# Optimization experiments

Hardware: AMD Instinct MI355X
Metric: run time of the kernel (lower is better)

The kernel has to match this reference:

```python
import jax, jax.numpy as jnp
import numpy as np

SCALE = 0.2  # init_kwargs: scale
EPS = 1e-12  # F.normalize default eps


def setup_inputs() -> dict:
    key = jax.random.key(0)
    x = jax.random.normal(key, (8, 2048, 512), dtype=jnp.float32)
    return {"x": x}


def reference(x):
    # x: [B, N, D]
    # F.normalize(x, dim=2): x / max(||x||_2, eps)
    norm = jnp.linalg.norm(x, axis=2, keepdims=True)
    x_norm = x / jnp.maximum(norm, EPS)
    # sim: [B, N, N] = x_norm @ x_norm^T, softmax over last dim
    sim = jnp.einsum('bnd,bmd->bnm', x_norm, x_norm)
    attn = jax.nn.softmax(sim, axis=2)
    # (1 + scale) * x - scale * attn @ x
    out = (1.0 + SCALE) * x - SCALE * jnp.einsum('bnm,bmd->bnd', attn, x)
    return out
```

## Files before the change

### kernel.cpp

```cpp
#include <hip/hip_runtime.h>
#include <stdint.h>

typedef unsigned short ushort_t;
typedef float f32x4 __attribute__((ext_vector_type(4)));
typedef short bf16x8 __attribute__((ext_vector_type(8)));
typedef unsigned short us8 __attribute__((ext_vector_type(8)));

#define BATCH 8
#define SEQ   2048
#define DIM   512
#define MBLK  64
#define KBLK  32
#define NIT   (SEQ / KBLK)

__device__ __forceinline__ ushort_t f2bf(float f) {
  union { float f; uint32_t u; } c; c.f = f;
  uint32_t u = c.u;
  uint32_t r = (u + 0x7FFFu + ((u >> 16) & 1u)) >> 16;
  return (ushort_t)r;
}
__device__ __forceinline__ uint32_t packbf(float a, float b) {
  return (uint32_t)f2bf(a) | ((uint32_t)f2bf(b) << 16);
}
__device__ __forceinline__ void gload_lds16(const void* g, void* l) {
  __builtin_amdgcn_global_load_lds(
      (const __attribute__((address_space(1))) unsigned int*)g,
      (__attribute__((address_space(3))) unsigned int*)l, 16, 0, 0);
}

__global__ void k_norm(const float* __restrict__ x, ushort_t* __restrict__ xn) {
  const int lane = threadIdx.x & 63;
  const int wid  = threadIdx.x >> 6;
  const size_t row = (size_t)blockIdx.x * 4 + wid;
  const float* xr = x + row * DIM;
  const float4 a = ((const float4*)xr)[lane * 2];
  const float4 b = ((const float4*)xr)[lane * 2 + 1];
  float ss = a.x*a.x + a.y*a.y + a.z*a.z + a.w*a.w
           + b.x*b.x + b.y*b.y + b.z*b.z + b.w*b.w;
#pragma unroll
  for (int m = 32; m >= 1; m >>= 1) ss += __shfl_xor(ss, m, 64);
  const float rn = 1.2011224087864498f / sqrtf(fmaxf(ss, 1e-30f));
  us8 o;
  o[0] = f2bf(a.x*rn); o[1] = f2bf(a.y*rn); o[2] = f2bf(a.z*rn); o[3] = f2bf(a.w*rn);
  o[4] = f2bf(b.x*rn); o[5] = f2bf(b.y*rn); o[6] = f2bf(b.z*rn); o[7] = f2bf(b.w*rn);
  *(us8*)(xn + row * DIM + lane * 8) = o;
}

__global__ void k_transpose(const float* __restrict__ x, ushort_t* __restrict__ vt) {
  __shared__ __align__(16) ushort_t tile[64][72];
  const int t   = threadIdx.x;
  const int bid = blockIdx.x;
  const int b   = bid >> 8;
  const int nt  = (bid >> 3) & 31;
  const int dt  = bid & 7;
  const size_t n0 = (size_t)nt * 64, d0 = (size_t)dt * 64;
  const float* xb = x + ((size_t)b * SEQ + n0) * DIM + d0;
#pragma unroll
  for (int p = 0; p < 4; ++p) {
    const int r  = p * 16 + (t >> 4);
    const int c4 = t & 15;
    const float4 v = *(const float4*)(xb + (size_t)r * DIM + c4 * 4);
    tile[c4*4+0][r] = f2bf(v.x);
    tile[c4*4+1][r] = f2bf(v.y);
    tile[c4*4+2][r] = f2bf(v.z);
    tile[c4*4+3][r] = f2bf(v.w);
  }
  __syncthreads();
  ushort_t* vb = vt + ((size_t)b * DIM + d0) * SEQ + n0;
  const int dd = t >> 2;
#pragma unroll
  for (int e = 0; e < 2; ++e) {
    const int c = (t & 3) * 2 + e;
    us8 v = *(const us8*)(&tile[dd][c * 8]);
    *(us8*)(vb + (size_t)dd * SEQ + c * 8) = v;
  }
}

__launch_bounds__(256, 1)
__global__ void k_attn(const ushort_t* __restrict__ xn, const ushort_t* __restrict__ vt,
                       const float* __restrict__ x, float* __restrict__ out) {
  extern __shared__ char smem[];
  ushort_t* Plds = (ushort_t*)smem;
  float* mstat = (float*)(smem + 4096);
  float* sstat = (float*)(smem + 4608);
  char* const Kb0 = smem + 8192;
  char* const Kb1 = smem + 8192 + 32768;
  char* const Vb0 = smem + 73728;
  char* const Vb1 = smem + 73728 + 32768;

  const int tid  = threadIdx.x;
  const int lane = tid & 63, wid = tid >> 6;
  const int mw = wid >> 1, nw = wid & 1;
  const int b  = blockIdx.x & 7, qt = blockIdx.x >> 3;
  const int q0 = qt * MBLK;
  const int ql = lane & 15, qg = lane >> 4;

  const ushort_t* xnb = xn + (size_t)b * SEQ * DIM;
  const ushort_t* vtb = vt + (size_t)b * DIM * SEQ;

  bf16x8 qreg[2][16];
#pragma unroll
  for (int h = 0; h < 2; ++h)
#pragma unroll
    for (int ks = 0; ks < 16; ++ks)
      qreg[h][ks] = *(const bf16x8*)(xnb + (size_t)(q0 + mw*32 + h*16 + ql) * DIM + ks*32 + qg*8);

  f32x4 acc[16][2];
#pragma unroll
  for (int ds = 0; ds < 16; ++ds)
#pragma unroll
    for (int m = 0; m < 2; ++m) acc[ds][m] = (f32x4){0.f, 0.f, 0.f, 0.f};
  float mrun0 = -3.0e38f, mrun1 = -3.0e38f, lrun0 = 0.f, lrun1 = 0.f;

  auto stage = [&](int it, char* Kb, char* Vb) {
    const int k0 = it * KBLK;
#pragma unroll
    for (int c = 0; c < 8; ++c) {
      const int idx = c * 256 + tid;
      const int kky = idx >> 6, dc = idx & 63;
      const ushort_t* g = xnb + (size_t)(k0 + kky) * DIM + ((dc ^ (kky & 7)) << 3);
      gload_lds16(g, Kb + (c * 256 + wid * 64) * 16);
    }
#pragma unroll
    for (int c = 0; c < 8; ++c) {
      const int idx = c * 256 + tid;
      const int d = idx >> 2, kc = idx & 3;
      const ushort_t* g = vtb + (size_t)d * SEQ + k0 + kc * 8;
      gload_lds16(g, Vb + (c * 256 + wid * 64) * 16);
    }
  };

  stage(0, Kb0, Vb0);
  asm volatile("s_waitcnt vmcnt(0)" ::: "memory");
  __builtin_amdgcn_s_barrier();
  asm volatile("" ::: "memory");

  for (int t = 0; t < NIT; ++t) {
    char* Kc = (t & 1) ? Kb1 : Kb0;
    char* Vc = (t & 1) ? Vb1 : Vb0;
    if (t + 1 < NIT) stage(t + 1, (t & 1) ? Kb0 : Kb1, (t & 1) ? Vb0 : Vb1);

    const int key = nw * 16 + ql;
    f32x4 c0 = (f32x4){0.f,0.f,0.f,0.f}, c1 = (f32x4){0.f,0.f,0.f,0.f};
#pragma unroll
    for (int ks = 0; ks < 16; ++ks) {
      const int chunk = ks * 4 + qg;
      bf16x8 af = *(const bf16x8*)(Kc + key * 1024 + ((chunk ^ (key & 7)) << 4));
      c0 = __builtin_amdgcn_mfma_f32_16x16x32_bf16(af, qreg[0][ks], c0, 0, 0, 0);
      c1 = __builtin_amdgcn_mfma_f32_16x16x32_bf16(af, qreg[1][ks], c1, 0, 0, 0);
    }
    float mt0 = fmaxf(fmaxf(c0[0], c0[1]), fmaxf(c0[2], c0[3]));
    float mt1 = fmaxf(fmaxf(c1[0], c1[1]), fmaxf(c1[2], c1[3]));
    mt0 = fmaxf(mt0, __shfl_xor(mt0, 16, 64)); mt0 = fmaxf(mt0, __shfl_xor(mt0, 32, 64));
    mt1 = fmaxf(mt1, __shfl_xor(mt1, 16, 64)); mt1 = fmaxf(mt1, __shfl_xor(mt1, 32, 64));
    if (lane < 32) mstat[(mw * 2 + nw) * 32 + lane] = (lane < 16) ? mt0 : mt1;
    asm volatile("s_waitcnt lgkmcnt(0)" ::: "memory");
    __builtin_amdgcn_s_barrier();
    asm volatile("" ::: "memory");
    const float mo0 = mstat[(mw * 2 + (nw ^ 1)) * 32 + ql];
    const float mo1 = mstat[(mw * 2 + (nw ^ 1)) * 32 + 16 + ql];
    const float mn0 = fmaxf(fmaxf(mt0, mo0), mrun0);
    const float mn1 = fmaxf(fmaxf(mt1, mo1), mrun1);
    const float sc0 = __builtin_amdgcn_exp2f(mrun0 - mn0);
    const float sc1 = __builtin_amdgcn_exp2f(mrun1 - mn1);
    mrun0 = mn0; mrun1 = mn1;
    f32x4 p0, p1;
#pragma unroll
    for (int j = 0; j < 4; ++j) {
      p0[j] = __builtin_amdgcn_exp2f(c0[j] - mn0);
      p1[j] = __builtin_amdgcn_exp2f(c1[j] - mn1);
    }
    float s0 = p0[0] + p0[1] + p0[2] + p0[3];
    float s1 = p1[0] + p1[1] + p1[2] + p1[3];
    s0 += __shfl_xor(s0, 16, 64); s0 += __shfl_xor(s0, 32, 64);
    s1 += __shfl_xor(s1, 16, 64); s1 += __shfl_xor(s1, 32, 64);
    if (lane < 32) sstat[(mw * 2 + nw) * 32 + lane] = (lane < 16) ? s0 : s1;
    {
      uint32_t* w0 = (uint32_t*)(Plds + (mw * 32 + ql) * 32 + nw * 16 + qg * 4);
      w0[0] = packbf(p0[0], p0[1]); w0[1] = packbf(p0[2], p0[3]);
      uint32_t* w1 = (uint32_t*)(Plds + (mw * 32 + 16 + ql) * 32 + nw * 16 + qg * 4);
      w1[0] = packbf(p1[0], p1[1]); w1[1] = packbf(p1[2], p1[3]);
    }
    asm volatile("s_waitcnt lgkmcnt(0)" ::: "memory");
    __builtin_amdgcn_s_barrier();
    asm volatile("" ::: "memory");
    const float so0 = sstat[(mw * 2 + (nw ^ 1)) * 32 + ql];
    const float so1 = sstat[(mw * 2 + (nw ^ 1)) * 32 + 16 + ql];
    lrun0 = lrun0 * sc0 + s0 + so0;
    lrun1 = lrun1 * sc1 + s1 + so1;
    float sca[2][4];
#pragma unroll
    for (int r = 0; r < 4; ++r) {
      sca[0][r] = __shfl(sc0, qg * 4 + r, 16);
      sca[1][r] = __shfl(sc1, qg * 4 + r, 16);
    }
#pragma unroll
    for (int ds = 0; ds < 16; ++ds)
#pragma unroll
      for (int m = 0; m < 2; ++m)
#pragma unroll
        for (int r = 0; r < 4; ++r) acc[ds][m][r] *= sca[m][r];
    bf16x8 pa0 = *(const bf16x8*)(Plds + (mw * 32 + ql) * 32 + qg * 8);
    bf16x8 pa1 = *(const bf16x8*)(Plds + (mw * 32 + 16 + ql) * 32 + qg * 8);
#pragma unroll
    for (int ds = 0; ds < 16; ++ds) {
      bf16x8 vb = *(const bf16x8*)(Vc + ((size_t)(nw * 256 + ds * 16 + ql) * 32 + qg * 8) * 2);
      acc[ds][0] = __builtin_amdgcn_mfma_f32_16x16x32_bf16(pa0, vb, acc[ds][0], 0, 0, 0);
      acc[ds][1] = __builtin_amdgcn_mfma_f32_16x16x32_bf16(pa1, vb, acc[ds][1], 0, 0, 0);
    }
    asm volatile("s_waitcnt vmcnt(0) lgkmcnt(0)" ::: "memory");
    __builtin_amdgcn_s_barrier();
    asm volatile("" ::: "memory");
  }

  float iv[2][4];
#pragma unroll
  for (int r = 0; r < 4; ++r) {
    iv[0][r] = 0.2f / __shfl(lrun0, qg * 4 + r, 16);
    iv[1][r] = 0.2f / __shfl(lrun1, qg * 4 + r, 16);
  }
  const float* xb = x   + ((size_t)b * SEQ + q0 + mw * 32) * DIM;
  float*       ob = out + ((size_t)b * SEQ + q0 + mw * 32) * DIM;
#pragma unroll
  for (int ds = 0; ds < 16; ++ds)
#pragma unroll
    for (int m = 0; m < 2; ++m)
#pragma unroll
      for (int r = 0; r < 4; ++r) {
        const int q = m * 16 + qg * 4 + r;
        const int d = nw * 256 + ds * 16 + ql;
        const float xv = xb[(size_t)q * DIM + d];
        ob[(size_t)q * DIM + d] = 1.2f * xv - iv[m][r] * acc[ds][m][r];
      }
}

extern "C" void kernel_launch(void* const* d_in, const int* in_sizes, int n_in,
                              void* d_out, int out_size, void* d_ws, size_t ws_size,
                              hipStream_t stream) {
  const float* x = (const float*)d_in[0];
  float* out = (float*)d_out;
  ushort_t* xn = (ushort_t*)d_ws;
  ushort_t* vt = (ushort_t*)((char*)d_ws + (size_t)BATCH * SEQ * DIM * 2);

  k_norm<<<BATCH * SEQ / 4, 256, 0, stream>>>(x, xn);
  k_transpose<<<BATCH * (SEQ / 64) * (DIM / 64), 256, 0, stream>>>(x, vt);
  (void)hipFuncSetAttribute((const void*)k_attn,
                            hipFuncAttributeMaxDynamicSharedMemorySize, 139264);
  k_attn<<<BATCH * SEQ / MBLK, 256, 139264, stream>>>(xn, vt, x, out);
}
```

Before: 273.9 us.

## Restructure attention kernel with 32x32 MFMA, split-D waves and fused prep

Merges the normalize and transpose kernels into one prep kernel that stages a 64-row tile in LDS. The attention kernel now runs 512 threads with 64-key blocks and 32x32x16 bf16 MFMAs. The QK dot product is split across two wave groups over D, and partial scores are combined through LDS. The running-max rescaling of online softmax is dropped, because the rows are unit-normalized and the scores are bounded, and V fragments are read straight from global memory into registers. The epilogue transposes accumulators through LDS for coalesced float4 output stores; in exchange it adds extra LDS traffic and barriers, and it relies on the scores never overflowing exp2.

```diff
diff --git a/kernel.cpp b/kernel.cpp
--- a/kernel.cpp
+++ b/kernel.cpp
@@ -2,22 +2,23 @@
 #include <stdint.h>
 
 typedef unsigned short ushort_t;
+typedef float f32x2 __attribute__((ext_vector_type(2)));
 typedef float f32x4 __attribute__((ext_vector_type(4)));
+typedef float f32x16 __attribute__((ext_vector_type(16)));
 typedef short bf16x8 __attribute__((ext_vector_type(8)));
 typedef unsigned short us8 __attribute__((ext_vector_type(8)));
 
 #define BATCH 8
 #define SEQ   2048
 #define DIM   512
-#define MBLK  64
-#define KBLK  32
+#define KBLK  64
 #define NIT   (SEQ / KBLK)
+#define LDS_TOTAL 156160
 
 __device__ __forceinline__ ushort_t f2bf(float f) {
   union { float f; uint32_t u; } c; c.f = f;
   uint32_t u = c.u;
-  uint32_t r = (u + 0x7FFFu + ((u >> 16) & 1u)) >> 16;
-  return (ushort_t)r;
+  return (ushort_t)((u + 0x7FFFu + ((u >> 16) & 1u)) >> 16);
 }
 __device__ __forceinline__ uint32_t packbf(float a, float b) {
   return (uint32_t)f2bf(a) | ((uint32_t)f2bf(b) << 16);
@@ -27,211 +28,194 @@
       (const __attribute__((address_space(1))) unsigned int*)g,
       (__attribute__((address_space(3))) unsigned int*)l, 16, 0, 0);
 }
-
-__global__ void k_norm(const float* __restrict__ x, ushort_t* __restrict__ xn) {
-  const int lane = threadIdx.x & 63;
-  const int wid  = threadIdx.x >> 6;
-  const size_t row = (size_t)blockIdx.x * 4 + wid;
-  const float* xr = x + row * DIM;
-  const float4 a = ((const float4*)xr)[lane * 2];
-  const float4 b = ((const float4*)xr)[lane * 2 + 1];
-  float ss = a.x*a.x + a.y*a.y + a.z*a.z + a.w*a.w
-           + b.x*b.x + b.y*b.y + b.z*b.z + b.w*b.w;
-#pragma unroll
-  for (int m = 32; m >= 1; m >>= 1) ss += __shfl_xor(ss, m, 64);
-  const float rn = 1.2011224087864498f / sqrtf(fmaxf(ss, 1e-30f));
-  us8 o;
-  o[0] = f2bf(a.x*rn); o[1] = f2bf(a.y*rn); o[2] = f2bf(a.z*rn); o[3] = f2bf(a.w*rn);
-  o[4] = f2bf(b.x*rn); o[5] = f2bf(b.y*rn); o[6] = f2bf(b.z*rn); o[7] = f2bf(b.w*rn);
-  *(us8*)(xn + row * DIM + lane * 8) = o;
-}
-
-__global__ void k_transpose(const float* __restrict__ x, ushort_t* __restrict__ vt) {
-  __shared__ __align__(16) ushort_t tile[64][72];
-  const int t   = threadIdx.x;
-  const int bid = blockIdx.x;
-  const int b   = bid >> 8;
-  const int nt  = (bid >> 3) & 31;
-  const int dt  = bid & 7;
-  const size_t n0 = (size_t)nt * 64, d0 = (size_t)dt * 64;
-  const float* xb = x + ((size_t)b * SEQ + n0) * DIM + d0;
-#pragma unroll
-  for (int p = 0; p < 4; ++p) {
-    const int r  = p * 16 + (t >> 4);
-    const int c4 = t & 15;
-    const float4 v = *(const float4*)(xb + (size_t)r * DIM + c4 * 4);
-    tile[c4*4+0][r] = f2bf(v.x);
-    tile[c4*4+1][r] = f2bf(v.y);
-    tile[c4*4+2][r] = f2bf(v.z);
-    tile[c4*4+3][r] = f2bf(v.w);
+#define WAIT_LGKM_BAR() { asm volatile("s_waitcnt lgkmcnt(0)" ::: "memory"); \
+  __builtin_amdgcn_s_barrier(); __builtin_amdgcn_sched_barrier(0); }
+#define WAIT_ALL_BAR()  { asm volatile("s_waitcnt vmcnt(0) lgkmcnt(0)" ::: "memory"); \
+  __builtin_amdgcn_s_barrier(); __builtin_amdgcn_sched_barrier(0); }
+
+__global__ void k_prep(const float* __restrict__ x, ushort_t* __restrict__ xn,
+                       ushort_t* __restrict__ vt) {
+  __shared__ __align__(16) ushort_t tile[64][512];
+  const int tid = threadIdx.x, lane = tid & 63, w = tid >> 6;
+  const int b = blockIdx.x >> 5, nt = blockIdx.x & 31;
+  const size_t row0 = (size_t)b * SEQ + (size_t)nt * 64;
+
+  for (int j = 0; j < 16; ++j) {
+    const int r = w * 16 + j;
+    const float* xr = x + (row0 + r) * DIM;
+    const float4 a  = ((const float4*)xr)[lane * 2];
+    const float4 bb = ((const float4*)xr)[lane * 2 + 1];
+    float ss = a.x*a.x + a.y*a.y + a.z*a.z + a.w*a.w
+             + bb.x*bb.x + bb.y*bb.y + bb.z*bb.z + bb.w*bb.w;
+#pragma unroll
+    for (int m = 32; m >= 1; m >>= 1) ss += __shfl_xor(ss, m, 64);
+    const float rn = 1.2011224087864498f / sqrtf(fmaxf(ss, 1e-24f));
+    us8 nrm, raw;
+    nrm[0]=f2bf(a.x*rn);  nrm[1]=f2bf(a.y*rn);  nrm[2]=f2bf(a.z*rn);  nrm[3]=f2bf(a.w*rn);
+    nrm[4]=f2bf(bb.x*rn); nrm[5]=f2bf(bb.y*rn); nrm[6]=f2bf(bb.z*rn); nrm[7]=f2bf(bb.w*rn);
+    raw[0]=f2bf(a.x);  raw[1]=f2bf(a.y);  raw[2]=f2bf(a.z);  raw[3]=f2bf(a.w);
+    raw[4]=f2bf(bb.x); raw[5]=f2bf(bb.y); raw[6]=f2bf(bb.z); raw[7]=f2bf(bb.w);
+    *(us8*)(xn + (row0 + r) * DIM + lane * 8) = nrm;
+    *(us8*)(&tile[r][lane * 8]) = raw;
   }
   __syncthreads();
-  ushort_t* vb = vt + ((size_t)b * DIM + d0) * SEQ + n0;
-  const int dd = t >> 2;
-#pragma unroll
-  for (int e = 0; e < 2; ++e) {
-    const int c = (t & 3) * 2 + e;
-    us8 v = *(const us8*)(&tile[dd][c * 8]);
-    *(us8*)(vb + (size_t)dd * SEQ + c * 8) = v;
-  }
-}
-
-__launch_bounds__(256, 1)
+#pragma unroll
+  for (int pass = 0; pass < 2; ++pass) {
+    const int d = pass * 256 + tid;
+    ushort_t* dst = vt + ((size_t)b * DIM + d) * SEQ + (size_t)nt * 64;
+#pragma unroll
+    for (int g = 0; g < 8; ++g) {
+      us8 v;
+#pragma unroll
+      for (int e = 0; e < 8; ++e) v[e] = tile[g * 8 + e][d];
+      *(us8*)(dst + g * 8) = v;
+    }
+  }
+}
+
+__launch_bounds__(512, 2)
 __global__ void k_attn(const ushort_t* __restrict__ xn, const ushort_t* __restrict__ vt,
                        const float* __restrict__ x, float* __restrict__ out) {
   extern __shared__ char smem[];
-  ushort_t* Plds = (ushort_t*)smem;
-  float* mstat = (float*)(smem + 4096);
-  float* sstat = (float*)(smem + 4608);
-  char* const Kb0 = smem + 8192;
-  char* const Kb1 = smem + 8192 + 32768;
-  char* const Vb0 = smem + 73728;
-  char* const Vb1 = smem + 73728 + 32768;
-
-  const int tid  = threadIdx.x;
-  const int lane = tid & 63, wid = tid >> 6;
-  const int mw = wid >> 1, nw = wid & 1;
-  const int b  = blockIdx.x & 7, qt = blockIdx.x >> 3;
-  const int q0 = qt * MBLK;
-  const int ql = lane & 15, qg = lane >> 4;
+  char* const Kb0 = smem;
+  char* const Kb1 = smem + 65536;
+  ushort_t* const P = (ushort_t*)(smem + 131072);
+  float* const Sp   = (float*)(smem + 139264);
+  float* const lsum = (float*)(smem + 155648);
+
+  const int tid = threadIdx.x;
+  const int lane = tid & 63, w = tid >> 6;
+  const int kw = w & 1, qw = (w >> 1) & 1, kd = w >> 2;
+  const int l31 = lane & 31, l5 = lane >> 5, l7 = lane & 7;
+  const int b = blockIdx.x & 7, qt0 = blockIdx.x >> 3;
+  const int q0 = qt0 * 64;
 
   const ushort_t* xnb = xn + (size_t)b * SEQ * DIM;
   const ushort_t* vtb = vt + (size_t)b * DIM * SEQ;
 
-  bf16x8 qreg[2][16];
-#pragma unroll
-  for (int h = 0; h < 2; ++h)
-#pragma unroll
-    for (int ks = 0; ks < 16; ++ks)
-      qreg[h][ks] = *(const bf16x8*)(xnb + (size_t)(q0 + mw*32 + h*16 + ql) * DIM + ks*32 + qg*8);
-
-  f32x4 acc[16][2];
-#pragma unroll
-  for (int ds = 0; ds < 16; ++ds)
-#pragma unroll
-    for (int m = 0; m < 2; ++m) acc[ds][m] = (f32x4){0.f, 0.f, 0.f, 0.f};
-  float mrun0 = -3.0e38f, mrun1 = -3.0e38f, lrun0 = 0.f, lrun1 = 0.f;
-
-  auto stage = [&](int it, char* Kb, char* Vb) {
-    const int k0 = it * KBLK;
-#pragma unroll
-    for (int c = 0; c < 8; ++c) {
-      const int idx = c * 256 + tid;
-      const int kky = idx >> 6, dc = idx & 63;
-      const ushort_t* g = xnb + (size_t)(k0 + kky) * DIM + ((dc ^ (kky & 7)) << 3);
-      gload_lds16(g, Kb + (c * 256 + wid * 64) * 16);
-    }
-#pragma unroll
-    for (int c = 0; c < 8; ++c) {
-      const int idx = c * 256 + tid;
-      const int d = idx >> 2, kc = idx & 3;
-      const ushort_t* g = vtb + (size_t)d * SEQ + k0 + kc * 8;
-      gload_lds16(g, Vb + (c * 256 + wid * 64) * 16);
-    }
-  };
-
-  stage(0, Kb0, Vb0);
+  bf16x8 qreg[16];
+#pragma unroll
+  for (int ks = 0; ks < 16; ++ks)
+    qreg[ks] = *(const bf16x8*)(xnb + (size_t)(q0 + qw * 32 + l31) * DIM
+                                + kd * 256 + ks * 16 + l5 * 8);
+
+  f32x16 acc[2][2] = {};
+  float plsum = 0.f;
+
+#pragma unroll
+  for (int i = 0; i < 8; ++i) {
+    const int row = w * 8 + i;
+    gload_lds16(xnb + (size_t)row * DIM + ((lane ^ i) << 3), Kb0 + row * 1024);
+  }
   asm volatile("s_waitcnt vmcnt(0)" ::: "memory");
   __builtin_amdgcn_s_barrier();
-  asm volatile("" ::: "memory");
+  __builtin_amdgcn_sched_barrier(0);
 
   for (int t = 0; t < NIT; ++t) {
-    char* Kc = (t & 1) ? Kb1 : Kb0;
-    char* Vc = (t & 1) ? Vb1 : Vb0;
-    if (t + 1 < NIT) stage(t + 1, (t & 1) ? Kb0 : Kb1, (t & 1) ? Vb0 : Vb1);
-
-    const int key = nw * 16 + ql;
-    f32x4 c0 = (f32x4){0.f,0.f,0.f,0.f}, c1 = (f32x4){0.f,0.f,0.f,0.f};
+    const int k0 = t * KBLK;
+    char* const Kc = (t & 1) ? Kb1 : Kb0;
+    char* const Kn = (t & 1) ? Kb0 : Kb1;
+
+    f32x16 accS = {};
+    const int arow = kw * 32 + l31;
 #pragma unroll
     for (int ks = 0; ks < 16; ++ks) {
-      const int chunk = ks * 4 + qg;
-      bf16x8 af = *(const bf16x8*)(Kc + key * 1024 + ((chunk ^ (key & 7)) << 4));
-      c0 = __builtin_amdgcn_mfma_f32_16x16x32_bf16(af, qreg[0][ks], c0, 0, 0, 0);
-      c1 = __builtin_amdgcn_mfma_f32_16x16x32_bf16(af, qreg[1][ks], c1, 0, 0, 0);
-    }
-    float mt0 = fmaxf(fmaxf(c0[0], c0[1]), fmaxf(c0[2], c0[3]));
-    float mt1 = fmaxf(fmaxf(c1[0], c1[1]), fmaxf(c1[2], c1[3]));
-    mt0 = fmaxf(mt0, __shfl_xor(mt0, 16, 64)); mt0 = fmaxf(mt0, __shfl_xor(mt0, 32, 64));
-    mt1 = fmaxf(mt1, __shfl_xor(mt1, 16, 64)); mt1 = fmaxf(mt1, __shfl_xor(mt1, 32, 64));
-    if (lane < 32) mstat[(mw * 2 + nw) * 32 + lane] = (lane < 16) ? mt0 : mt1;
-    asm volatile("s_waitcnt lgkmcnt(0)" ::: "memory");
-    __builtin_amdgcn_s_barrier();
-    asm volatile("" ::: "memory");
-    const float mo0 = mstat[(mw * 2 + (nw ^ 1)) * 32 + ql];
-    const float mo1 = mstat[(mw * 2 + (nw ^ 1)) * 32 + 16 + ql];
-    const float mn0 = fmaxf(fmaxf(mt0, mo0), mrun0);
-    const float mn1 = fmaxf(fmaxf(mt1, mo1), mrun1);
-    const float sc0 = __builtin_amdgcn_exp2f(mrun0 - mn0);
-    const float sc1 = __builtin_amdgcn_exp2f(mrun1 - mn1);
-    mrun0 = mn0; mrun1 = mn1;
-    f32x4 p0, p1;
-#pragma unroll
-    for (int j = 0; j < 4; ++j) {
-      p0[j] = __builtin_amdgcn_exp2f(c0[j] - mn0);
-      p1[j] = __builtin_amdgcn_exp2f(c1[j] - mn1);
-    }
-    float s0 = p0[0] + p0[1] + p0[2] + p0[3];
-    float s1 = p1[0] + p1[1] + p1[2] + p1[3];
-    s0 += __shfl_xor(s0, 16, 64); s0 += __shfl_xor(s0, 32, 64);
-    s1 += __shfl_xor(s1, 16, 64); s1 += __shfl_xor(s1, 32, 64);
-    if (lane < 32) sstat[(mw * 2 + nw) * 32 + lane] = (lane < 16) ? s0 : s1;
-    {
-      uint32_t* w0 = (uint32_t*)(Plds + (mw * 32 + ql) * 32 + nw * 16 + qg * 4);
-      w0[0] = packbf(p0[0], p0[1]); w0[1] = packbf(p0[2], p0[3]);
-      uint32_t* w1 = (uint32_t*)(Plds + (mw * 32 + 16 + ql) * 32 + nw * 16 + qg * 4);
-      w1[0] = packbf(p1[0], p1[1]); w1[1] = packbf(p1[2], p1[3]);
-    }
-    asm volatile("s_waitcnt lgkmcnt(0)" ::: "memory");
-    __builtin_amdgcn_s_barrier();
-    asm volatile("" ::: "memory");
-    const float so0 = sstat[(mw * 2 + (nw ^ 1)) * 32 + ql];
-    const float so1 = sstat[(mw * 2 + (nw ^ 1)) * 32 + 16 + ql];
-    lrun0 = lrun0 * sc0 + s0 + so0;
-    lrun1 = lrun1 * sc1 + s1 + so1;
-    float sca[2][4];
-#pragma unroll
-    for (int r = 0; r < 4; ++r) {
-      sca[0][r] = __shfl(sc0, qg * 4 + r, 16);
-      sca[1][r] = __shfl(sc1, qg * 4 + r, 16);
-    }
-#pragma unroll
-    for (int ds = 0; ds < 16; ++ds)
-#pragma unroll
-      for (int m = 0; m < 2; ++m)
-#pragma unroll
-        for (int r = 0; r < 4; ++r) acc[ds][m][r] *= sca[m][r];
-    bf16x8 pa0 = *(const bf16x8*)(Plds + (mw * 32 + ql) * 32 + qg * 8);
-    bf16x8 pa1 = *(const bf16x8*)(Plds + (mw * 32 + 16 + ql) * 32 + qg * 8);
-#pragma unroll
-    for (int ds = 0; ds < 16; ++ds) {
-      bf16x8 vb = *(const bf16x8*)(Vc + ((size_t)(nw * 256 + ds * 16 + ql) * 32 + qg * 8) * 2);
-      acc[ds][0] = __builtin_amdgcn_mfma_f32_16x16x32_bf16(pa0, vb, acc[ds][0], 0, 0, 0);
-      acc[ds][1] = __builtin_amdgcn_mfma_f32_16x16x32_bf16(pa1, vb, acc[ds][1], 0, 0, 0);
-    }
-    asm volatile("s_waitcnt vmcnt(0) lgkmcnt(0)" ::: "memory");
-    __builtin_amdgcn_s_barrier();
-    asm volatile("" ::: "memory");
-  }
-
-  float iv[2][4];
-#pragma unroll
-  for (int r = 0; r < 4; ++r) {
-    iv[0][r] = 0.2f / __shfl(lrun0, qg * 4 + r, 16);
-    iv[1][r] = 0.2f / __shfl(lrun1, qg * 4 + r, 16);
-  }
-  const float* xb = x   + ((size_t)b * SEQ + q0 + mw * 32) * DIM;
-  float*       ob = out + ((size_t)b * SEQ + q0 + mw * 32) * DIM;
-#pragma unroll
-  for (int ds = 0; ds < 16; ++ds)
-#pragma unroll
-    for (int m = 0; m < 2; ++m)
-#pragma unroll
-      for (int r = 0; r < 4; ++r) {
-        const int q = m * 16 + qg * 4 + r;
-        const int d = nw * 256 + ds * 16 + ql;
-        const float xv = xb[(size_t)q * DIM + d];
-        ob[(size_t)q * DIM + d] = 1.2f * xv - iv[m][r] * acc[ds][m][r];
-      }
+      const int c = kd * 32 + ks * 2 + l5;
+      bf16x8 af = *(const bf16x8*)(Kc + arow * 1024 + ((c ^ l7) << 4));
+      accS = __builtin_amdgcn_mfma_f32_32x32x16_bf16(af, qreg[ks], accS, 0, 0, 0);
+    }
+
+    if (kd) {
+      float* tile = Sp + (kw * 2 + qw) * 1024 + l31 * 32;
+#pragma unroll
+      for (int j = 0; j < 8; ++j) {
+        const int u = (j & 1) + 4 * (j >> 1) + 2 * l5;
+        f32x2 v = { accS[2 * j], accS[2 * j + 1] };
+        *(f32x2*)(tile + ((u ^ l7) << 1)) = v;
+      }
+    }
+    WAIT_LGKM_BAR();
+
+    bf16x8 vv[2][4];
+#pragma unroll
+    for (int dt = 0; dt < 2; ++dt)
+#pragma unroll
+      for (int ks = 0; ks < 4; ++ks)
+        vv[dt][ks] = *(const bf16x8*)(vtb + (size_t)(w * 64 + dt * 32 + l31) * SEQ
+                                      + k0 + ks * 16 + l5 * 8);
+
+    if (!kd) {
+      const float* tile = Sp + (kw * 2 + qw) * 1024 + l31 * 32;
+      uint32_t* prow = (uint32_t*)(P + (qw * 32 + l31) * 64);
+#pragma unroll
+      for (int j = 0; j < 8; ++j) {
+        const int u = (j & 1) + 4 * (j >> 1) + 2 * l5;
+        f32x2 o = *(const f32x2*)(tile + ((u ^ l7) << 1));
+        float p0 = __builtin_amdgcn_exp2f(accS[2 * j]     + o[0]);
+        float p1 = __builtin_amdgcn_exp2f(accS[2 * j + 1] + o[1]);
+        plsum += p0 + p1;
+        const int chunk = (kw * 4 + (j >> 1)) ^ l7;
+        prow[chunk * 4 + (j & 1) + 2 * l5] = packbf(p0, p1);
+      }
+    } else if (t + 1 < NIT) {
+      const int sid = w - 4;
+#pragma unroll
+      for (int i = 0; i < 16; ++i) {
+        const int row = sid * 16 + i;
+        gload_lds16(xnb + (size_t)(k0 + KBLK + row) * DIM + ((lane ^ (i & 7)) << 3),
+                    Kn + row * 1024);
+      }
+    }
+    WAIT_LGKM_BAR();
+
+#pragma unroll
+    for (int qt = 0; qt < 2; ++qt) {
+#pragma unroll
+      for (int ks = 0; ks < 4; ++ks) {
+        const int c = (ks * 2 + l5) ^ l7;
+        bf16x8 pa = *(const bf16x8*)(P + (qt * 32 + l31) * 64 + c * 8);
+        acc[qt][0] = __builtin_amdgcn_mfma_f32_32x32x16_bf16(pa, vv[0][ks], acc[qt][0], 0, 0, 0);
+        acc[qt][1] = __builtin_amdgcn_mfma_f32_32x32x16_bf16(pa, vv[1][ks], acc[qt][1], 0, 0, 0);
+      }
+    }
+    WAIT_ALL_BAR();
+  }
+
+  if (!kd) {
+    plsum += __shfl_xor(plsum, 32, 64);
+    if (lane < 32) lsum[kw * 64 + qw * 32 + lane] = plsum;
+  }
+  float* obuf = (float*)smem;
+#pragma unroll
+  for (int qt = 0; qt < 2; ++qt)
+#pragma unroll
+    for (int dt = 0; dt < 2; ++dt) {
+      const int d = w * 64 + dt * 32 + l31;
+#pragma unroll
+      for (int r = 0; r < 16; ++r) {
+        const int q = qt * 32 + (r & 3) + 8 * (r >> 2) + 4 * l5;
+        const int c = (d >> 2) ^ (q & 7);
+        obuf[q * 512 + c * 4 + (d & 3)] = acc[qt][dt][r];
+      }
+    }
+  WAIT_LGKM_BAR();
+
+  const int q = tid >> 3, seg = tid & 7;
+  const float s = 0.2f / (lsum[q] + lsum[64 + q]);
+  const size_t grow = ((size_t)b * SEQ + q0 + q) * DIM;
+#pragma unroll
+  for (int i = 0; i < 16; ++i) {
+    const int c = seg * 16 + i;
+    const int cs = c ^ (q & 7);
+    f32x4 a = *(const f32x4*)(obuf + q * 512 + cs * 4);
+    const float4 xv = *(const float4*)(x + grow + c * 4);
+    float4 o;
+    o.x = 1.2f * xv.x - s * a[0];
+    o.y = 1.2f * xv.y - s * a[1];
+    o.z = 1.2f * xv.z - s * a[2];
+    o.w = 1.2f * xv.w - s * a[3];
+    *(float4*)(out + grow + c * 4) = o;
+  }
 }
 
 extern "C" void kernel_launch(void* const* d_in, const int* in_sizes, int n_in,
@@ -242,9 +226,8 @@
   ushort_t* xn = (ushort_t*)d_ws;
   ushort_t* vt = (ushort_t*)((char*)d_ws + (size_t)BATCH * SEQ * DIM * 2);
 
-  k_norm<<<BATCH * SEQ / 4, 256, 0, stream>>>(x, xn);
-  k_transpose<<<BATCH * (SEQ / 64) * (DIM / 64), 256, 0, stream>>>(x, vt);
+  k_prep<<<BATCH * (SEQ / 64), 256, 0, stream>>>(x, xn, vt);
   (void)hipFuncSetAttribute((const void*)k_attn,
-                            hipFuncAttributeMaxDynamicSharedMemorySize, 139264);
-  k_attn<<<BATCH * SEQ / MBLK, 256, 139264, stream>>>(xn, vt, x, out);
-}
+                            hipFuncAttributeMaxDynamicSharedMemorySize, LDS_TOTAL);
+  k_attn<<<BATCH * SEQ / 64, 512, LDS_TOTAL, stream>>>(xn, vt, x, out);
+}
```

Measured after the change: 226.4 us. 1.21x faster.
